# Optimization experiments

Measured on AMD Instinct MI355X. Metric: run time of the kernel, lower is better.

## Reference

```python
import jax, jax.numpy as jnp
import numpy as np

N = 50000
NUM_NEIGHBORS = 16
E = N * NUM_NEIGHBORS
NDIM_IN, EDIM, NDIM_OUT = 128, 64, 128


def setup_inputs() -> dict:
    key = jax.random.key(0)
    k1, k2, k3, k4, k5, k6, k7 = jax.random.split(key, 7)
    nfeats = jax.random.normal(k1, (N, 1, NDIM_IN), dtype=jnp.float32)
    efeats = jax.random.normal(k2, (E, 1, EDIM), dtype=jnp.float32)
    W_msg = jax.random.normal(k3, (NDIM_OUT, NDIM_IN + EDIM), dtype=jnp.float32) * 0.05
    b_msg = jax.random.normal(k4, (NDIM_OUT,), dtype=jnp.float32) * 0.05
    W_apply = jax.random.normal(k5, (NDIM_OUT, NDIM_IN + NDIM_OUT), dtype=jnp.float32) * 0.05
    b_apply = jax.random.normal(k6, (NDIM_OUT,), dtype=jnp.float32) * 0.05
    src_idx = jax.random.randint(k7, (E,), 0, N, dtype=jnp.int32)
    # sampled graph: each node is the destination of exactly NUM_NEIGHBORS edges
    dst_idx = jnp.repeat(jnp.arange(N, dtype=jnp.int32), NUM_NEIGHBORS)
    return {"nfeats": nfeats, "efeats": efeats, "W_msg": W_msg, "b_msg": b_msg,
            "W_apply": W_apply, "b_apply": b_apply, "src_idx": src_idx, "dst_idx": dst_idx}


def reference(nfeats, efeats, W_msg, b_msg, W_apply, b_apply, src_idx, dst_idx):
    n = nfeats.shape[0]
    # message: W_msg(cat([src_h, edge_h], -1))  -> [E, 1, ndim_out]
    src_h = nfeats[src_idx]                                   # [E,1,Din] gather
    msg_in = jnp.concatenate([src_h, efeats], axis=-1)        # [E,1,Din+Edim]
    m = jnp.einsum('eid,od->eio', msg_in, W_msg) + b_msg      # [E,1,Dout]
    # mean aggregation over incoming edges per destination node
    msum = jax.ops.segment_sum(m[:, 0, :], dst_idx, num_segments=n)   # [N,Dout]
    cnt = jax.ops.segment_sum(jnp.ones((m.shape[0],), m.dtype), dst_idx, num_segments=n)
    h_neigh = (msum / jnp.maximum(cnt, 1.0)[:, None])[:, None, :]     # [N,1,Dout]
    # apply: relu(W_apply(cat([nfeats, h_neigh], -1)))
    app_in = jnp.concatenate([nfeats, h_neigh], axis=-1)      # [N,1,Din+Dout]
    h_new = jax.nn.relu(jnp.einsum('nid,od->nio', app_in, W_apply) + b_apply)
    return h_new
```

## Files before the change

### kernel.cpp

```cpp
#include <hip/hip_runtime.h>

#define N_NODES 50000
#define NN 16
#define K_FUSED 320
#define NP 50048

typedef __attribute__((ext_vector_type(8))) short bfrag8;
typedef __attribute__((ext_vector_type(4))) float facc4;

__device__ __forceinline__ unsigned short f2bf(float f) {
    unsigned int u = __builtin_bit_cast(unsigned int, f);
    u = (u + 0x7fffu + ((u >> 16) & 1u)) >> 16;
    return (unsigned short)u;
}
__device__ __forceinline__ float bf2f(unsigned int u16) {
    return __builtin_bit_cast(float, u16 << 16);
}
__device__ __forceinline__ unsigned int pack2(unsigned short lo, unsigned short hi) {
    return (unsigned int)lo | ((unsigned int)hi << 16);
}

__global__ void wfuse_kernel(const float* __restrict__ W_msg,
                             const float* __restrict__ b_msg,
                             const float* __restrict__ W_apply,
                             const float* __restrict__ b_apply,
                             unsigned short* __restrict__ Wf,
                             float* __restrict__ bias_f) {
    __shared__ float sWa[128];
    const int o = blockIdx.x;
    const int tid = threadIdx.x;
    if (tid < 128) sWa[tid] = W_apply[o * 256 + 128 + tid];
    __syncthreads();
    if (tid < 128) Wf[o * K_FUSED + tid] = f2bf(W_apply[o * 256 + tid]);
    if (tid < 192) {
        float acc = 0.f;
        #pragma unroll 8
        for (int p = 0; p < 128; ++p) acc += sWa[p] * W_msg[p * 192 + tid];
        Wf[o * K_FUSED + 128 + tid] = f2bf(acc);
    } else if (tid == 192) {
        float acc = b_apply[o];
        for (int p = 0; p < 128; ++p) acc += sWa[p] * b_msg[p];
        bias_f[o] = acc;
    }
}

__global__ __launch_bounds__(256)
void cvt_kernel(const float* __restrict__ nfeats,
                unsigned short* __restrict__ X,
                unsigned short* __restrict__ nbf) {
    const int idx = blockIdx.x * 256 + threadIdx.x;
    const int n = idx >> 5, d = (idx & 31) * 4;
    const float4 v = *(const float4*)(nfeats + (long)n * 128 + d);
    uint2 p;
    p.x = pack2(f2bf(v.x), f2bf(v.y));
    p.y = pack2(f2bf(v.z), f2bf(v.w));
    *(uint2*)(nbf + (long)n * 128 + d) = p;
    *(uint2*)(X + (long)n * K_FUSED + d) = p;
}

__global__ __launch_bounds__(256)
void prep_kernel(const unsigned short* __restrict__ nbf,
                 const float* __restrict__ efeats,
                 const int* __restrict__ src_idx,
                 unsigned short* __restrict__ X) {
    const int wave = threadIdx.x >> 6;
    const int lane = threadIdx.x & 63;
    const int n = blockIdx.x * 4 + wave;
    if (n >= N_NODES) return;
    const long e0 = (long)n * NN;

    const int myidx = src_idx[e0 + (lane & 15)];

    float s0 = 0.f, s1 = 0.f;
    #pragma unroll
    for (int j = 0; j < NN; ++j) {
        const int src = __builtin_amdgcn_readlane(myidx, j);
        const unsigned int v =
            *(const unsigned int*)(nbf + (long)src * 128 + 2 * lane);
        s0 += bf2f(v & 0xffffu);
        s1 += bf2f(v >> 16);
    }

    const float4* eb = (const float4*)(efeats + e0 * 64);
    float t0 = 0.f, t1 = 0.f, t2 = 0.f, t3 = 0.f;
    #pragma unroll
    for (int it = 0; it < 4; ++it) {
        const float4 v = eb[it * 64 + lane];
        t0 += v.x; t1 += v.y; t2 += v.z; t3 += v.w;
    }
    #pragma unroll
    for (int off = 16; off <= 32; off <<= 1) {
        t0 += __shfl_xor(t0, off);
        t1 += __shfl_xor(t1, off);
        t2 += __shfl_xor(t2, off);
        t3 += __shfl_xor(t3, off);
    }

    const float inv = 1.f / 16.f;
    unsigned short* row = X + (long)n * K_FUSED;
    ((unsigned int*)(row + 128))[lane] =
        pack2(f2bf(s0 * inv), f2bf(s1 * inv));
    if (lane < 16) {
        uint2 p;
        p.x = pack2(f2bf(t0 * inv), f2bf(t1 * inv));
        p.y = pack2(f2bf(t2 * inv), f2bf(t3 * inv));
        *(uint2*)(row + 256 + 4 * lane) = p;
    }
}

__global__ __launch_bounds__(512)
void apply_kernel(const unsigned short* __restrict__ X,
                  const uint4* __restrict__ WfQ,
                  const float* __restrict__ bias_f,
                  float* __restrict__ out) {
    __shared__ uint4 ldsW[64 * 41];
    const int bx = blockIdx.x;
    const int mblk = bx >> 1;
    const int nhalf = bx & 1;
    const int tid = threadIdx.x;

    #pragma unroll
    for (int i = tid; i < 64 * 40; i += 512) {
        const int r = i / 40, q = i - r * 40;
        ldsW[r * 41 + q] = WfQ[(nhalf * 64 + r) * 40 + q];
    }
    __syncthreads();

    const int wave = tid >> 6, lane = tid & 63;
    const int quad = lane >> 4, mcol = lane & 15;
    const int node0 = mblk * 128 + wave * 16;
    const char* arow = (const char*)(X + (long)(node0 + mcol) * K_FUSED);
    const char* ldsB = (const char*)ldsW;

    facc4 acc[4] = {};
    #pragma unroll
    for (int ks = 0; ks < 10; ++ks) {
        const uint4 av = *(const uint4*)(arow + ks * 64 + quad * 16);
        const bfrag8 a = __builtin_bit_cast(bfrag8, av);
        #pragma unroll
        for (int t = 0; t < 4; ++t) {
            const int nrow = t * 16 + mcol;
            const uint4 bv = *(const uint4*)(ldsB + nrow * 656 + ks * 64 + quad * 16);
            const bfrag8 b = __builtin_bit_cast(bfrag8, bv);
            acc[t] = __builtin_amdgcn_mfma_f32_16x16x32_bf16(a, b, acc[t], 0, 0, 0);
        }
    }

    #pragma unroll
    for (int t = 0; t < 4; ++t) {
        const int ocol = nhalf * 64 + t * 16 + mcol;
        const float bb = bias_f[ocol];
        #pragma unroll
        for (int r = 0; r < 4; ++r) {
            const int node = node0 + quad * 4 + r;
            if (node < N_NODES) {
                const float v = acc[t][r] + bb;
                out[(long)node * 128 + ocol] = v > 0.f ? v : 0.f;
            }
        }
    }
}

extern "C" void kernel_launch(void* const* d_in, const int* in_sizes, int n_in,
                              void* d_out, int out_size, void* d_ws, size_t ws_size,
                              hipStream_t stream) {
    const float* nfeats  = (const float*)d_in[0];
    const float* efeats  = (const float*)d_in[1];
    const float* W_msg   = (const float*)d_in[2];
    const float* b_msg   = (const float*)d_in[3];
    const float* W_apply = (const float*)d_in[4];
    const float* b_apply = (const float*)d_in[5];
    const int*   src_idx = (const int*)d_in[6];
    float* out = (float*)d_out;

    char* ws = (char*)d_ws;
    unsigned short* Wf     = (unsigned short*)ws;
    float*          bias_f = (float*)(ws + 81920);
    unsigned short* X      = (unsigned short*)(ws + 82432);
    unsigned short* nbf    = (unsigned short*)(ws + 82432 + (size_t)NP * K_FUSED * 2);

    wfuse_kernel<<<128, 256, 0, stream>>>(W_msg, b_msg, W_apply, b_apply, Wf, bias_f);
    cvt_kernel<<<(N_NODES * 32) / 256, 256, 0, stream>>>(nfeats, X, nbf);
    prep_kernel<<<(N_NODES + 3) / 4, 256, 0, stream>>>(nbf, efeats, src_idx, X);
    apply_kernel<<<(NP / 128) * 2, 512, 0, stream>>>(X, (const uint4*)Wf, bias_f, out);
}
```

Baseline: 352.2 us.

## Store X and fused weights in MFMA fragment order, widen apply tiles

X and the fused weight matrix are now written in a pre-swizzled layout that matches the 16x16x32 bf16 MFMA fragment order, so each lane loads a contiguous uint4. The apply kernel copies the whole 128-column weight into LDS and each wave computes two 16-row tiles against all 8 output tiles, which gives more reuse of the B fragments and removes the duplicate A loads across column halves. The bounds check is dropped from prep_kernel; because there are 12500 blocks of 4 nodes, n never exceeds N. Weight staging doubles to 80KB of LDS, and 64 accumulators per lane push up register use and may lower occupancy.

```diff
diff --git a/kernel.cpp b/kernel.cpp
--- a/kernel.cpp
+++ b/kernel.cpp
@@ -4,6 +4,7 @@
 #define NN 16
 #define K_FUSED 320
 #define NP 50048
+#define NTILES (NP / 16)
 
 typedef __attribute__((ext_vector_type(8))) short bfrag8;
 typedef __attribute__((ext_vector_type(4))) float facc4;
@@ -20,23 +21,32 @@
     return (unsigned int)lo | ((unsigned int)hi << 16);
 }
 
+
 __global__ void wfuse_kernel(const float* __restrict__ W_msg,
                              const float* __restrict__ b_msg,
                              const float* __restrict__ W_apply,
                              const float* __restrict__ b_apply,
-                             unsigned short* __restrict__ Wf,
+                             unsigned short* __restrict__ WfF,
                              float* __restrict__ bias_f) {
     __shared__ float sWa[128];
     const int o = blockIdx.x;
     const int tid = threadIdx.x;
     if (tid < 128) sWa[tid] = W_apply[o * 256 + 128 + tid];
     __syncthreads();
-    if (tid < 128) Wf[o * K_FUSED + tid] = f2bf(W_apply[o * 256 + tid]);
+    if (tid < 128) {
+        const int k = tid;
+        const long C = ((long)(((k >> 5) * 8 + (o >> 4)) * 64 +
+                               ((k >> 3) & 3) * 16 + (o & 15)) << 3) + (k & 7);
+        WfF[C] = f2bf(W_apply[o * 256 + k]);
+    }
     if (tid < 192) {
         float acc = 0.f;
         #pragma unroll 8
         for (int p = 0; p < 128; ++p) acc += sWa[p] * W_msg[p * 192 + tid];
-        Wf[o * K_FUSED + 128 + tid] = f2bf(acc);
+        const int k = 128 + tid;
+        const long C = ((long)(((k >> 5) * 8 + (o >> 4)) * 64 +
+                               ((k >> 3) & 3) * 16 + (o & 15)) << 3) + (k & 7);
+        WfF[C] = f2bf(acc);
     } else if (tid == 192) {
         float acc = b_apply[o];
         for (int p = 0; p < 128; ++p) acc += sWa[p] * b_msg[p];
@@ -46,7 +56,7 @@
 
 __global__ __launch_bounds__(256)
 void cvt_kernel(const float* __restrict__ nfeats,
-                unsigned short* __restrict__ X,
+                unsigned short* __restrict__ Xf,
                 unsigned short* __restrict__ nbf) {
     const int idx = blockIdx.x * 256 + threadIdx.x;
     const int n = idx >> 5, d = (idx & 31) * 4;
@@ -55,18 +65,19 @@
     p.x = pack2(f2bf(v.x), f2bf(v.y));
     p.y = pack2(f2bf(v.z), f2bf(v.w));
     *(uint2*)(nbf + (long)n * 128 + d) = p;
-    *(uint2*)(X + (long)n * K_FUSED + d) = p;
+    const long C = ((long)(((n >> 4) * 10 + (d >> 5)) * 64 +
+                           ((d >> 3) & 3) * 16 + (n & 15)) << 3) + (d & 7);
+    *(uint2*)(Xf + C) = p;
 }
 
 __global__ __launch_bounds__(256)
 void prep_kernel(const unsigned short* __restrict__ nbf,
                  const float* __restrict__ efeats,
                  const int* __restrict__ src_idx,
-                 unsigned short* __restrict__ X) {
+                 unsigned short* __restrict__ Xf) {
     const int wave = threadIdx.x >> 6;
     const int lane = threadIdx.x & 63;
     const int n = blockIdx.x * 4 + wave;
-    if (n >= N_NODES) return;
     const long e0 = (long)n * NN;
 
     const int myidx = src_idx[e0 + (lane & 15)];
@@ -97,65 +108,69 @@
     }
 
     const float inv = 1.f / 16.f;
-    unsigned short* row = X + (long)n * K_FUSED;
-    ((unsigned int*)(row + 128))[lane] =
-        pack2(f2bf(s0 * inv), f2bf(s1 * inv));
+    const int tile = n >> 4, row = n & 15;
+    {
+        const int kb = 4 + (lane >> 4);
+        const int quad = (lane >> 2) & 3;
+        const int j = (2 * lane) & 7;
+        const long C = ((long)((tile * 10 + kb) * 64 + quad * 16 + row) << 3) + j;
+        *(unsigned int*)(Xf + C) = pack2(f2bf(s0 * inv), f2bf(s1 * inv));
+    }
     if (lane < 16) {
+        const int kb = 8 + (lane >> 3);
+        const int quad = (lane >> 1) & 3;
+        const int j = 4 * (lane & 1);
+        const long C = ((long)((tile * 10 + kb) * 64 + quad * 16 + row) << 3) + j;
         uint2 p;
         p.x = pack2(f2bf(t0 * inv), f2bf(t1 * inv));
         p.y = pack2(f2bf(t2 * inv), f2bf(t3 * inv));
-        *(uint2*)(row + 256 + 4 * lane) = p;
-    }
-}
-
-__global__ __launch_bounds__(512)
-void apply_kernel(const unsigned short* __restrict__ X,
-                  const uint4* __restrict__ WfQ,
+        *(uint2*)(Xf + C) = p;
+    }
+}
+
+__global__ __launch_bounds__(256)
+void apply_kernel(const uint4* __restrict__ Xf,
+                  const uint4* __restrict__ WfF,
                   const float* __restrict__ bias_f,
                   float* __restrict__ out) {
-    __shared__ uint4 ldsW[64 * 41];
-    const int bx = blockIdx.x;
-    const int mblk = bx >> 1;
-    const int nhalf = bx & 1;
+    __shared__ uint4 ldsW[5120];
     const int tid = threadIdx.x;
-
-    #pragma unroll
-    for (int i = tid; i < 64 * 40; i += 512) {
-        const int r = i / 40, q = i - r * 40;
-        ldsW[r * 41 + q] = WfQ[(nhalf * 64 + r) * 40 + q];
-    }
+    #pragma unroll
+    for (int i = tid; i < 5120; i += 256) ldsW[i] = WfF[i];
     __syncthreads();
 
     const int wave = tid >> 6, lane = tid & 63;
     const int quad = lane >> 4, mcol = lane & 15;
-    const int node0 = mblk * 128 + wave * 16;
-    const char* arow = (const char*)(X + (long)(node0 + mcol) * K_FUSED);
-    const char* ldsB = (const char*)ldsW;
-
-    facc4 acc[4] = {};
+    const int tile0 = blockIdx.x * 8 + wave * 2;
+
+    facc4 acc0[8] = {}, acc1[8] = {};
     #pragma unroll
     for (int ks = 0; ks < 10; ++ks) {
-        const uint4 av = *(const uint4*)(arow + ks * 64 + quad * 16);
-        const bfrag8 a = __builtin_bit_cast(bfrag8, av);
+        const bfrag8 a0 = __builtin_bit_cast(bfrag8, Xf[(tile0 * 10 + ks) * 64 + lane]);
+        const bfrag8 a1 = __builtin_bit_cast(bfrag8, Xf[((tile0 + 1) * 10 + ks) * 64 + lane]);
         #pragma unroll
-        for (int t = 0; t < 4; ++t) {
-            const int nrow = t * 16 + mcol;
-            const uint4 bv = *(const uint4*)(ldsB + nrow * 656 + ks * 64 + quad * 16);
-            const bfrag8 b = __builtin_bit_cast(bfrag8, bv);
-            acc[t] = __builtin_amdgcn_mfma_f32_16x16x32_bf16(a, b, acc[t], 0, 0, 0);
+        for (int t = 0; t < 8; ++t) {
+            const bfrag8 b = __builtin_bit_cast(bfrag8, ldsW[(ks * 8 + t) * 64 + lane]);
+            acc0[t] = __builtin_amdgcn_mfma_f32_16x16x32_bf16(a0, b, acc0[t], 0, 0, 0);
+            acc1[t] = __builtin_amdgcn_mfma_f32_16x16x32_bf16(a1, b, acc1[t], 0, 0, 0);
         }
     }
 
     #pragma unroll
-    for (int t = 0; t < 4; ++t) {
-        const int ocol = nhalf * 64 + t * 16 + mcol;
+    for (int t = 0; t < 8; ++t) {
+        const int ocol = t * 16 + mcol;
         const float bb = bias_f[ocol];
         #pragma unroll
         for (int r = 0; r < 4; ++r) {
-            const int node = node0 + quad * 4 + r;
-            if (node < N_NODES) {
-                const float v = acc[t][r] + bb;
-                out[(long)node * 128 + ocol] = v > 0.f ? v : 0.f;
+            const int n0 = tile0 * 16 + quad * 4 + r;
+            const int n1 = n0 + 16;
+            if (n0 < N_NODES) {
+                const float v = acc0[t][r] + bb;
+                out[(long)n0 * 128 + ocol] = v > 0.f ? v : 0.f;
+            }
+            if (n1 < N_NODES) {
+                const float v = acc1[t][r] + bb;
+                out[(long)n1 * 128 + ocol] = v > 0.f ? v : 0.f;
             }
         }
     }
@@ -174,13 +189,14 @@
     float* out = (float*)d_out;
 
     char* ws = (char*)d_ws;
-    unsigned short* Wf     = (unsigned short*)ws;
+    unsigned short* WfF    = (unsigned short*)ws;
     float*          bias_f = (float*)(ws + 81920);
-    unsigned short* X      = (unsigned short*)(ws + 82432);
+    unsigned short* Xf     = (unsigned short*)(ws + 82432);
     unsigned short* nbf    = (unsigned short*)(ws + 82432 + (size_t)NP * K_FUSED * 2);
 
-    wfuse_kernel<<<128, 256, 0, stream>>>(W_msg, b_msg, W_apply, b_apply, Wf, bias_f);
-    cvt_kernel<<<(N_NODES * 32) / 256, 256, 0, stream>>>(nfeats, X, nbf);
-    prep_kernel<<<(N_NODES + 3) / 4, 256, 0, stream>>>(nbf, efeats, src_idx, X);
-    apply_kernel<<<(NP / 128) * 2, 512, 0, stream>>>(X, (const uint4*)Wf, bias_f, out);
-}
+    wfuse_kernel<<<128, 256, 0, stream>>>(W_msg, b_msg, W_apply, b_apply, WfF, bias_f);
+    cvt_kernel<<<(N_NODES * 32) / 256, 256, 0, stream>>>(nfeats, Xf, nbf);
+    prep_kernel<<<(N_NODES + 3) / 4, 256, 0, stream>>>(nbf, efeats, src_idx, Xf);
+    apply_kernel<<<NP / 128, 256, 0, stream>>>((const uint4*)Xf, (const uint4*)WfF,
+                                               bias_f, out);
+}
```

Result: slower. 359.6 us (+2.1%).
